# Performance work log

Hardware: AMD Instinct MI355X
Metric: run time of the kernel (lower is better)

Reference implementation:

```python
import jax, jax.numpy as jnp
import numpy as np
import math

B, S, E, H = 2, 2048, 1024, 16
D = E // H
# neuromodulator levels (deterministic branch choices)
NA, ACH, DA = 0.5, 0.5, -0.5

def setup_inputs() -> dict:
    key = jax.random.key(0)
    ks = jax.random.split(key, 12)
    xav = lambda k, i, o: jax.random.uniform(k, (i, o), jnp.float32, -1.0, 1.0) * math.sqrt(6.0 / (i + o))
    return {
        'query': jax.random.normal(ks[0], (B, S, E), jnp.float32),
        'key':   jax.random.normal(ks[1], (B, S, E), jnp.float32),
        'value': jax.random.normal(ks[2], (B, S, E), jnp.float32),
        'Wq': xav(ks[3], E, E), 'bq': jnp.zeros((E,), jnp.float32),
        'Wk': xav(ks[4], E, E), 'bk': jnp.zeros((E,), jnp.float32),
        'Wv': xav(ks[5], E, E), 'bv': jnp.zeros((E,), jnp.float32),
        'Wo': xav(ks[6], E, E), 'bo': jnp.zeros((E,), jnp.float32),
        'time_scales': jnp.ones((H,), jnp.float32),
    }

def reference(query, key, value, Wq, bq, Wk, bk, Wv, bv, Wo, bo, time_scales):
    # projections -> [B, H, S, D]
    q = (query @ Wq + bq).reshape(B, S, H, D).transpose(0, 2, 1, 3)
    k = (key   @ Wk + bk).reshape(B, S, H, D).transpose(0, 2, 1, 3)
    v = (value @ Wv + bv).reshape(B, S, H, D).transpose(0, 2, 1, 3)
    # per-head time-scale on keys
    k = k * time_scales[None, :, None, None]
    scores = jnp.einsum('bhtd,bhsd->bhts', q, k) / math.sqrt(D)
    # noradrenaline: temperature scaling
    temperature = 1.0 / (1.0 + NA * 0.5)
    scores = scores / temperature
    # acetylcholine: boost diagonal
    diag = jnp.eye(S, dtype=scores.dtype)[None, None]
    scores = scores * (1.0 + ACH * 0.3 * diag)
    kk = max(1, int(S * 0.2))
    topv = jax.lax.top_k(scores, kk)[0]          # [B,H,S,kk]
    min_topk = topv[..., -1:]                     # kth largest
    mask = (scores >= min_topk).astype(scores.dtype)
    scores = scores * (1.0 + (-DA) * 0.3 * mask)
    attn = jax.nn.softmax(scores, axis=-1)
    out = jnp.einsum('bhts,bhsd->bhtd', attn, v)
    out = out.transpose(0, 2, 1, 3).reshape(B, S, E)
    out = out @ Wo + bo
    return out
```

## Files before the change

kernel.cpp:

```cpp
#include <hip/hip_runtime.h>
#include <cstdint>
#include <cstddef>

#define BB 2
#define SS 2048
#define EE 1024
#define HH 16
#define DH 64
#define KKSEL 409
#define QT 16
#define PST 136

typedef __attribute__((ext_vector_type(8))) short bf16x8;
typedef __attribute__((ext_vector_type(4))) float f32x4;
typedef unsigned short ushort_t;

__device__ __forceinline__ unsigned short f2bf(float f){
    unsigned u = __float_as_uint(f);
    u += 0x7fffu + ((u >> 16) & 1u);
    return (unsigned short)(u >> 16);
}
__device__ __forceinline__ float bf2f(unsigned short h){
    return __uint_as_float(((unsigned)h) << 16);
}
__device__ __forceinline__ unsigned sortkey(float f){
    unsigned u = __float_as_uint(f);
    return (u & 0x80000000u) ? ~u : (u | 0x80000000u);
}
__device__ __forceinline__ float inv_sortkey(unsigned k){
    unsigned u = (k & 0x80000000u) ? (k & 0x7fffffffu) : ~k;
    return __uint_as_float(u);
}
__device__ __forceinline__ void split8(const float* f, bf16x8& h, bf16x8& l){
    #pragma unroll
    for (int j = 0; j < 8; ++j){
        ushort_t hh = f2bf(f[j]);
        h[j] = (short)hh;
        l[j] = (short)f2bf(f[j] - bf2f(hh));
    }
}
__device__ __forceinline__ void gload_lds16(const ushort_t* g, ushort_t* l){
    __builtin_amdgcn_global_load_lds(
        (const __attribute__((address_space(1))) void*)g,
        (__attribute__((address_space(3))) void*)l, 16, 0, 0);
}

struct CvtArgs {
    const float* W[4];
    ushort_t* H[4];
    ushort_t* L[4];
};

__global__ __launch_bounds__(256) void convert_wt4(CvtArgs a)
{
    __shared__ float T[64][65];
    const int z = blockIdx.z;
    const float* __restrict__ W = a.W[z];
    ushort_t* __restrict__ Ht = a.H[z];
    ushort_t* __restrict__ Lt = a.L[z];

    const int tid = threadIdx.x;
    const int ty = tid >> 4, tx = tid & 15;
    const int n0 = blockIdx.x * 64, k0 = blockIdx.y * 64;
    #pragma unroll
    for (int i = 0; i < 4; ++i){
        const int kl = ty + i * 16;
        float4 w = *(const float4*)&W[(size_t)(k0 + kl) * EE + n0 + tx * 4];
        T[kl][tx*4 + 0] = w.x; T[kl][tx*4 + 1] = w.y;
        T[kl][tx*4 + 2] = w.z; T[kl][tx*4 + 3] = w.w;
    }
    __syncthreads();
    #pragma unroll
    for (int i = 0; i < 4; ++i){
        const int nl = ty + i * 16;
        ushort4 h, l;
        ushort_t* hp = &h.x; ushort_t* lp = &l.x;
        #pragma unroll
        for (int j = 0; j < 4; ++j){
            const float v = T[tx*4 + j][nl];
            ushort_t hh = f2bf(v);
            hp[j] = hh;
            lp[j] = f2bf(v - bf2f(hh));
        }
        const size_t o = (size_t)(n0 + nl) * EE + k0 + tx * 4;
        *(ushort4*)&Ht[o] = h;
        *(ushort4*)&Lt[o] = l;
    }
}

template<int MODE>
__device__ __forceinline__ void gemm_body(
        const float* __restrict__ X,
        const ushort_t* __restrict__ Wth, const ushort_t* __restrict__ Wtl,
        const float* __restrict__ bias, const float* __restrict__ ts,
        float* __restrict__ OutF, ushort_t* __restrict__ OutH,
        ushort_t* __restrict__ OutL, ushort_t* buf, int bx, int by)
{
    const int tid  = threadIdx.x;
    const int lane = tid & 63, wave = tid >> 6;
    const int c16  = lane & 15, qd = lane >> 4;
    const int m0 = by * 128, n0 = bx * 64;
    const int wm = (wave >> 1) * 64, wn = (wave & 1) * 32;
    const int lrow = tid >> 1, lkg = (tid & 1) * 16;

    f32x4 acc[8];
    #pragma unroll
    for (int i = 0; i < 8; ++i) acc[i] = (f32x4){0.f,0.f,0.f,0.f};

    const float* Xr = X + (size_t)(m0 + lrow) * EE + lkg;

    const size_t wofs = (size_t)(n0 + wave*16 + (lane >> 2)) * EE + (lane & 3) * 8;
    const ushort_t* Wh = Wth + wofs;
    const ushort_t* Wl = Wtl + wofs;

    for (int k0 = 0; k0 < EE; k0 += 32){
        gload_lds16(Wh + k0, buf + 8192  + wave*512);
        gload_lds16(Wl + k0, buf + 10240 + wave*512);
        {
            float fx[16];
            const float* xp = Xr + k0;
            *(float4*)&fx[0]  = *(const float4*)&xp[0];
            *(float4*)&fx[4]  = *(const float4*)&xp[4];
            *(float4*)&fx[8]  = *(const float4*)&xp[8];
            *(float4*)&fx[12] = *(const float4*)&xp[12];
            bf16x8 h0, l0, h1, l1;
            split8(fx, h0, l0); split8(fx + 8, h1, l1);
            *(bf16x8*)&buf[lrow*32 + lkg]           = h0;
            *(bf16x8*)&buf[lrow*32 + lkg + 8]       = h1;
            *(bf16x8*)&buf[4096 + lrow*32 + lkg]    = l0;
            *(bf16x8*)&buf[4096 + lrow*32 + lkg+8]  = l1;
        }
        __syncthreads();

        const ushort_t* A0 = buf;
        const ushort_t* A1 = buf + 4096;
        const ushort_t* B0 = buf + 8192;
        const ushort_t* B1 = buf + 10240;
        bf16x8 afh[4], afl[4], bfh[2], bfl[2];
        #pragma unroll
        for (int i = 0; i < 4; ++i){
            afh[i] = *(const bf16x8*)&A0[(wm + i*16 + c16)*32 + qd*8];
            afl[i] = *(const bf16x8*)&A1[(wm + i*16 + c16)*32 + qd*8];
        }
        #pragma unroll
        for (int j = 0; j < 2; ++j){
            bfh[j] = *(const bf16x8*)&B0[(wn + j*16 + c16)*32 + qd*8];
            bfl[j] = *(const bf16x8*)&B1[(wn + j*16 + c16)*32 + qd*8];
        }
        if (MODE == 2){
            #pragma unroll
            for (int ma = 0; ma < 4; ++ma){
                #pragma unroll
                for (int nb = 0; nb < 2; ++nb){
                    const int id = ma*2 + nb;
                    acc[id] = __builtin_amdgcn_mfma_f32_16x16x32_bf16(afh[ma], bfh[nb], acc[id], 0,0,0);
                    acc[id] = __builtin_amdgcn_mfma_f32_16x16x32_bf16(afh[ma], bfl[nb], acc[id], 0,0,0);
                    acc[id] = __builtin_amdgcn_mfma_f32_16x16x32_bf16(afl[ma], bfh[nb], acc[id], 0,0,0);
                }
            }
        } else {
            #pragma unroll
            for (int na = 0; na < 2; ++na){
                #pragma unroll
                for (int mb = 0; mb < 4; ++mb){
                    const int id = na*4 + mb;
                    acc[id] = __builtin_amdgcn_mfma_f32_16x16x32_bf16(bfh[na], afh[mb], acc[id], 0,0,0);
                    acc[id] = __builtin_amdgcn_mfma_f32_16x16x32_bf16(bfh[na], afl[mb], acc[id], 0,0,0);
                    acc[id] = __builtin_amdgcn_mfma_f32_16x16x32_bf16(bfl[na], afh[mb], acc[id], 0,0,0);
                }
            }
        }
        if (k0 + 32 < EE) __syncthreads();
    }

    if (MODE == 3){
        #pragma unroll
        for (int na = 0; na < 2; ++na){
            const int ng = n0 + wn + na*16 + qd*4;
            float4 b4 = *(const float4*)&bias[ng];
            const float bb[4] = {b4.x, b4.y, b4.z, b4.w};
            #pragma unroll
            for (int mb = 0; mb < 4; ++mb){
                const int mg = m0 + wm + mb*16 + c16;
                const f32x4 av = acc[na*4 + mb];
                float4 o;
                o.x = av[0] + bb[0]; o.y = av[1] + bb[1];
                o.z = av[2] + bb[2]; o.w = av[3] + bb[3];
                *(float4*)&OutF[(size_t)mg * EE + ng] = o;
            }
        }
    } else if (MODE == 0){
        #pragma unroll
        for (int na = 0; na < 2; ++na){
            const int ng = n0 + wn + na*16 + qd*4;
            const int h = ng >> 6, d0 = ng & 63;
            float4 b4 = *(const float4*)&bias[ng];
            const float bb[4] = {b4.x, b4.y, b4.z, b4.w};
            #pragma unroll
            for (int mb = 0; mb < 4; ++mb){
                const int mg = m0 + wm + mb*16 + c16;
                const int bi = mg >> 11, s = mg & (SS - 1);
                const f32x4 av = acc[na*4 + mb];
                ushort4 hv, lv;
                ushort_t* hp = &hv.x; ushort_t* lp = &lv.x;
                #pragma unroll
                for (int r = 0; r < 4; ++r){
                    const float v = av[r] + bb[r];
                    ushort_t hh = f2bf(v);
                    hp[r] = hh;
                    lp[r] = f2bf(v - bf2f(hh));
                }
                const size_t o = (((size_t)(bi * HH + h)) * SS + s) * DH + d0;
                *(ushort4*)&OutH[o] = hv;
                *(ushort4*)&OutL[o] = lv;
            }
        }
    } else if (MODE == 1){
        #pragma unroll
        for (int na = 0; na < 2; ++na){
            const int ng = n0 + wn + na*16 + qd*4;
            const int h = ng >> 6, d0 = ng & 63;
            const float tsc = ts[h];
            float4 b4 = *(const float4*)&bias[ng];
            const float bb[4] = {b4.x, b4.y, b4.z, b4.w};
            #pragma unroll
            for (int mb = 0; mb < 4; ++mb){
                const int mg = m0 + wm + mb*16 + c16;
                const int bi = mg >> 11, s = mg & (SS - 1);
                const f32x4 av = acc[na*4 + mb];
                ushort4 hv;
                ushort_t* hp = &hv.x;
                #pragma unroll
                for (int r = 0; r < 4; ++r)
                    hp[r] = f2bf((av[r] + bb[r]) * tsc);
                *(ushort4*)&OutH[(((size_t)(bi * HH + h)) * SS + s) * DH + d0] = hv;
            }
        }
    } else {
        #pragma unroll
        for (int ma = 0; ma < 4; ++ma){
            const int mg = m0 + wm + ma*16 + qd*4;
            const int bi = mg >> 11, s0 = mg & (SS - 1);
            #pragma unroll
            for (int nb = 0; nb < 2; ++nb){
                const int ng = n0 + wn + nb*16 + c16;
                const int h = ng >> 6, d = ng & 63;
                const float bv = bias[ng];
                const f32x4 av = acc[ma*2 + nb];
                ushort4 hv;
                ushort_t* hp = &hv.x;
                #pragma unroll
                for (int r = 0; r < 4; ++r) hp[r] = f2bf(av[r] + bv);
                *(ushort4*)&OutH[(((size_t)(bi * HH + h)) * DH + d) * SS + s0] = hv;
            }
        }
    }
}

__device__ __forceinline__ void panel_swizzle(int& bx, int& by){
    const int lin = blockIdx.x + 16 * blockIdx.y;
    const int xcd = lin & 7, idx = lin >> 3;
    bx = idx & 15;
    by = (xcd << 2) | (idx >> 4);
}

__global__ __launch_bounds__(256) void gemm_qkv(
        const float* __restrict__ q, const float* __restrict__ k,
        const float* __restrict__ v,
        const ushort_t* __restrict__ Wqh, const ushort_t* __restrict__ Wql,
        const ushort_t* __restrict__ Wkh, const ushort_t* __restrict__ Wkl,
        const ushort_t* __restrict__ Wvh, const ushort_t* __restrict__ Wvl,
        const float* __restrict__ bq, const float* __restrict__ bk,
        const float* __restrict__ bv, const float* __restrict__ ts,
        ushort_t* __restrict__ Qh, ushort_t* __restrict__ Ql,
        ushort_t* __restrict__ Kh, ushort_t* __restrict__ Vth)
{
    __shared__ ushort_t buf[12288];
    int bx, by;
    panel_swizzle(bx, by);
    const int z = blockIdx.z;
    if (z == 0)
        gemm_body<0>(q, Wqh, Wql, bq, nullptr, nullptr, Qh, Ql, buf, bx, by);
    else if (z == 1)
        gemm_body<1>(k, Wkh, Wkl, bk, ts, nullptr, Kh, nullptr, buf, bx, by);
    else
        gemm_body<2>(v, Wvh, Wvl, bv, nullptr, nullptr, Vth, nullptr, buf, bx, by);
}

__global__ __launch_bounds__(256) void gemm_out(
        const float* __restrict__ X,
        const ushort_t* __restrict__ Wth, const ushort_t* __restrict__ Wtl,
        const float* __restrict__ bias, float* __restrict__ OutF)
{
    __shared__ ushort_t buf[12288];
    int bx, by;
    panel_swizzle(bx, by);
    gemm_body<3>(X, Wth, Wtl, bias, nullptr, OutF, nullptr, nullptr, buf, bx, by);
}

__global__ __launch_bounds__(512, 4) void attn_kernel(
        const ushort_t* __restrict__ Qh, const ushort_t* __restrict__ Ql,
        const ushort_t* __restrict__ Khi, const ushort_t* __restrict__ Vth,
        float* __restrict__ AO)
{
    __shared__ __align__(16) char uni[65536];
    __shared__ float wsums[8][16];
    __shared__ unsigned thr16[16];

    const int tid  = threadIdx.x;
    const int lane = tid & 63;
    const int wave = tid >> 6;
    const int qd   = lane >> 4;
    const int c16  = lane & 15;
    const unsigned Bx = blockIdx.x;
    const int xcd  = Bx & 7;
    const int qq   = Bx >> 3;
    const int tile = qq & 127;
    const int bh   = (qq >> 7) * 8 + xcd;
    const int t0   = tile * QT;
    const int wbase = wave * 256;

    bf16x8 qh[2], ql[2];
    {
        const size_t qbase = ((size_t)bh * SS + t0 + c16) * DH;
        #pragma unroll
        for (int kc = 0; kc < 2; ++kc){
            qh[kc] = *(const bf16x8*)&Qh[qbase + kc*32 + qd*8];
            ql[kc] = *(const bf16x8*)&Ql[qbase + kc*32 + qd*8];
        }
    }

    f32x4 acc[16];
    const ushort_t* Kh = Khi + (size_t)bh * SS * DH;
    #pragma unroll
    for (int t = 0; t < 16; ++t){
        f32x4 a = {0.f, 0.f, 0.f, 0.f};
        const int srow = wbase + t*16 + c16;
        const ushort_t* kp = Kh + (size_t)srow * DH + qd*8;
        #pragma unroll
        for (int kc = 0; kc < 2; ++kc){
            bf16x8 kh = *(const bf16x8*)(kp + kc*32);
            a = __builtin_amdgcn_mfma_f32_16x16x32_bf16(qh[kc], kh, a, 0, 0, 0);
            a = __builtin_amdgcn_mfma_f32_16x16x32_bf16(ql[kc], kh, a, 0, 0, 0);
        }
        acc[t] = a;
    }

    #pragma unroll
    for (int t = 0; t < 16; ++t){
        const int colg = wbase + t*16 + c16;
        #pragma unroll
        for (int r = 0; r < 4; ++r){
            float v = acc[t][r] * 0.15625f;
            if (colg == t0 + qd*4 + r) v *= 1.15f;
            acc[t][r] = __uint_as_float(sortkey(v));
        }
    }

    float* ex = (float*)uni;
    #pragma unroll
    for (int half = 0; half < 2; ++half){
        if ((qd >> 1) == half){
            const int rl = (qd & 1) * 4;
            #pragma unroll
            for (int t = 0; t < 16; ++t)
                #pragma unroll
                for (int r = 0; r < 4; ++r)
                    ex[(rl + r) * SS + wbase + t*16 + c16] = acc[t][r];
        }
        __syncthreads();
        unsigned cand[32];
        #pragma unroll
        for (int j = 0; j < 32; ++j)
            cand[j] = __float_as_uint(ex[wave * SS + lane + 64*j]);
        unsigned kmn = cand[0], kmx = cand[0];
        #pragma unroll
        for (int j = 1; j < 32; ++j){
            kmn = (cand[j] < kmn) ? cand[j] : kmn;
            kmx = (cand[j] > kmx) ? cand[j] : kmx;
        }
        #pragma unroll
        for (int off = 1; off < 64; off <<= 1){
            const unsigned on = (unsigned)__shfl_xor((int)kmn, off, 64);
            const unsigned ox = (unsigned)__shfl_xor((int)kmx, off, 64);
            kmn = (on < kmn) ? on : kmn;
            kmx = (ox > kmx) ? ox : kmx;
        }
        unsigned lo = kmn, hi = kmx + 1u;
        #pragma unroll 1
        for (int it = 0; it < 32 && (hi - lo) > 1u; ++it){
            const unsigned mid = lo + ((hi - lo) >> 1);
            int c = 0;
            #pragma unroll
            for (int j = 0; j < 32; ++j){
                int pc;
                asm("v_cmp_le_u32 vcc, %1, %2\n\t"
                    "s_bcnt1_i32_b64 %0, vcc"
                    : "=s"(pc) : "s"(mid), "v"(cand[j]) : "vcc");
                c += pc;
            }
            if (c == KKSEL){ lo = mid; break; }
            if (c > KKSEL) lo = mid; else hi = mid;
        }
        if (lane == 0) thr16[half*8 + wave] = lo;
        __syncthreads();
    }

    unsigned thr[4];
    #pragma unroll
    for (int r = 0; r < 4; ++r) thr[r] = thr16[qd*4 + r];
    float psum[4] = {0.f, 0.f, 0.f, 0.f};
    #pragma unroll
    for (int t = 0; t < 16; ++t){
        #pragma unroll
        for (int r = 0; r < 4; ++r){
            const unsigned key = __float_as_uint(acc[t][r]);
            float s = inv_sortkey(key);
            s *= (key >= thr[r]) ? 1.15f : 1.0f;
            const float e = __expf(s);
            acc[t][r] = e;
            psum[r] += e;
        }
    }
    #pragma unroll
    for (int off = 1; off <= 8; off <<= 1){
        #pragma unroll
        for (int r = 0; r < 4; ++r) psum[r] += __shfl_xor(psum[r], off, 64);
    }
    if (c16 == 0){
        #pragma unroll
        for (int r = 0; r < 4; ++r) wsums[wave][qd*4 + r] = psum[r];
    }
    __syncthreads();
    float pinv[4];
    #pragma unroll
    for (int r = 0; r < 4; ++r){
        const int row = qd*4 + r;
        float s = 0.f;
        #pragma unroll
        for (int w = 0; w < 8; ++w) s += wsums[w][row];
        pinv[r] = 1.f / s;
    }

    const ushort_t* Vh = Vth + (size_t)bh * DH * SS;
    ushort_t* pw = (ushort_t*)uni + wave * (QT * PST);
    f32x4 oacc[4];
    #pragma unroll
    for (int dt = 0; dt < 4; ++dt) oacc[dt] = (f32x4){0.f, 0.f, 0.f, 0.f};

    #pragma unroll
    for (int half = 0; half < 2; ++half){
        #pragma unroll
        for (int tt = 0; tt < 8; ++tt){
            const int t = half*8 + tt;
            #pragma unroll
            for (int r = 0; r < 4; ++r)
                pw[(qd*4 + r) * PST + tt*16 + c16] = f2bf(acc[t][r] * pinv[r]);
        }
        #pragma unroll
        for (int kc = 0; kc < 4; ++kc){
            bf16x8 pf = *(const bf16x8*)&pw[c16 * PST + kc*32 + qd*8];
            const int sbase = wbase + half*128 + kc*32 + qd*8;
            #pragma unroll
            for (int dt = 0; dt < 4; ++dt){
                const int d = dt*16 + c16;
                bf16x8 vh = *(const bf16x8*)(Vh + (size_t)d * SS + sbase);
                oacc[dt] = __builtin_amdgcn_mfma_f32_16x16x32_bf16(pf, vh, oacc[dt], 0, 0, 0);
            }
        }
    }

    __syncthreads();
    float* red = (float*)uni;
    #pragma unroll
    for (int dt = 0; dt < 4; ++dt)
        #pragma unroll
        for (int r = 0; r < 4; ++r)
            red[(wave*16 + qd*4 + r) * 65 + dt*16 + c16] = oacc[dt][r];
    __syncthreads();

    const int b = bh >> 4, h = bh & 15;
    {
        const int r  = tid >> 5;
        const int c2 = (tid & 31) * 2;
        float s0 = 0.f, s1 = 0.f;
        #pragma unroll
        for (int w = 0; w < 8; ++w){
            s0 += red[(w*16 + r) * 65 + c2];
            s1 += red[(w*16 + r) * 65 + c2 + 1];
        }
        float2 o; o.x = s0; o.y = s1;
        *(float2*)&AO[((size_t)b * SS + t0 + r) * EE + h*DH + c2] = o;
    }
}

extern "C" void kernel_launch(void* const* d_in, const int* in_sizes, int n_in,
                              void* d_out, int out_size, void* d_ws, size_t ws_size,
                              hipStream_t stream)
{
    const float* query = (const float*)d_in[0];
    const float* key   = (const float*)d_in[1];
    const float* value = (const float*)d_in[2];
    const float* Wq    = (const float*)d_in[3];
    const float* bq    = (const float*)d_in[4];
    const float* Wk    = (const float*)d_in[5];
    const float* bk    = (const float*)d_in[6];
    const float* Wv    = (const float*)d_in[7];
    const float* bv    = (const float*)d_in[8];
    const float* Wo    = (const float*)d_in[9];
    const float* bo    = (const float*)d_in[10];
    const float* ts    = (const float*)d_in[11];
    float* out = (float*)d_out;
    char* w = (char*)d_ws;

    const size_t MB = 1u << 20;
    ushort_t* Qh  = (ushort_t*)(w + 0 * MB);
    ushort_t* Ql  = (ushort_t*)(w + 8 * MB);
    ushort_t* Kh  = (ushort_t*)(w + 16 * MB);
    ushort_t* Vth = (ushort_t*)(w + 24 * MB);
    float*    AOw = (float*)   (w + 32 * MB);
    ushort_t* Wqh = (ushort_t*)(w + 32 * MB);
    ushort_t* Wql = (ushort_t*)(w + 34 * MB);
    ushort_t* Wkh = (ushort_t*)(w + 36 * MB);
    ushort_t* Wkl = (ushort_t*)(w + 38 * MB);
    ushort_t* Wvh = (ushort_t*)(w + 40 * MB);
    ushort_t* Wvl = (ushort_t*)(w + 42 * MB);
    ushort_t* Woh = (ushort_t*)(w + 48 * MB);
    ushort_t* Wol = (ushort_t*)(w + 50 * MB);

    CvtArgs ca;
    ca.W[0] = Wq;  ca.W[1] = Wk;  ca.W[2] = Wv;  ca.W[3] = Wo;
    ca.H[0] = Wqh; ca.H[1] = Wkh; ca.H[2] = Wvh; ca.H[3] = Woh;
    ca.L[0] = Wql; ca.L[1] = Wkl; ca.L[2] = Wvl; ca.L[3] = Wol;

    hipLaunchKernelGGL(convert_wt4, dim3(16, 16, 4), dim3(256), 0, stream, ca);
    hipLaunchKernelGGL(gemm_qkv, dim3(16, 32, 3), dim3(256), 0, stream,
                       query, key, value, Wqh, Wql, Wkh, Wkl, Wvh, Wvl,
                       bq, bk, bv, ts, Qh, Ql, Kh, Vth);
    hipLaunchKernelGGL(attn_kernel, dim3(BB * HH * (SS / QT)), dim3(512), 0, stream,
                       Qh, Ql, Kh, Vth, AOw);
    hipLaunchKernelGGL(gemm_out, dim3(16, 32), dim3(256), 0, stream,
                       AOw, Woh, Wol, bo, out);
}
```

Baseline: 663.0 us.

## Pre-split GEMM activations to bf16 hi/lo and stream them via direct LDS loads

Adds a separate pass that converts query/key/value into bf16 high/low pairs. The attention kernel now writes its output as hi/lo pairs as well. Both GEMMs then load activations with asynchronous global-to-LDS copies instead of loading fp32 into registers, splitting, and writing to LDS. This removes per-tile conversion work and the register round-trip from the GEMM inner loop, but adds an extra kernel and extra global traffic for the converted copies. It also reuses the Xq workspace region for the attention output.

```diff
diff --git a/kernel.cpp b/kernel.cpp
--- a/kernel.cpp
+++ b/kernel.cpp
@@ -88,9 +88,31 @@
     }
 }
 
+struct CvtX {
+    const float* X[3];
+    ushort_t* H[3];
+    ushort_t* L[3];
+};
+
+__global__ __launch_bounds__(256) void convert_x3(CvtX a)
+{
+    const int z = blockIdx.z;
+    const float* __restrict__ X = a.X[z];
+    ushort_t* __restrict__ Hd = a.H[z];
+    ushort_t* __restrict__ Ld = a.L[z];
+    const size_t i = ((size_t)blockIdx.x * 256 + threadIdx.x) * 8;
+    float fx[8];
+    *(float4*)&fx[0] = *(const float4*)&X[i];
+    *(float4*)&fx[4] = *(const float4*)&X[i + 4];
+    bf16x8 h, l;
+    split8(fx, h, l);
+    *(bf16x8*)&Hd[i] = h;
+    *(bf16x8*)&Ld[i] = l;
+}
+
 template<int MODE>
 __device__ __forceinline__ void gemm_body(
-        const float* __restrict__ X,
+        const ushort_t* __restrict__ Xh, const ushort_t* __restrict__ Xl,
         const ushort_t* __restrict__ Wth, const ushort_t* __restrict__ Wtl,
         const float* __restrict__ bias, const float* __restrict__ ts,
         float* __restrict__ OutF, ushort_t* __restrict__ OutH,
@@ -101,35 +123,24 @@
     const int c16  = lane & 15, qd = lane >> 4;
     const int m0 = by * 128, n0 = bx * 64;
     const int wm = (wave >> 1) * 64, wn = (wave & 1) * 32;
-    const int lrow = tid >> 1, lkg = (tid & 1) * 16;
 
     f32x4 acc[8];
     #pragma unroll
     for (int i = 0; i < 8; ++i) acc[i] = (f32x4){0.f,0.f,0.f,0.f};
 
-    const float* Xr = X + (size_t)(m0 + lrow) * EE + lkg;
-
-    const size_t wofs = (size_t)(n0 + wave*16 + (lane >> 2)) * EE + (lane & 3) * 8;
-    const ushort_t* Wh = Wth + wofs;
-    const ushort_t* Wl = Wtl + wofs;
+    const int seg0 = wave * 2, seg1 = seg0 + 1;
+    const int rl = lane >> 2, kl = (lane & 3) * 8;
+    const size_t xofs0 = (size_t)(m0 + seg0*16 + rl) * EE + kl;
+    const size_t xofs1 = (size_t)(m0 + seg1*16 + rl) * EE + kl;
+    const size_t wofs = (size_t)(n0 + wave*16 + rl) * EE + kl;
 
     for (int k0 = 0; k0 < EE; k0 += 32){
-        gload_lds16(Wh + k0, buf + 8192  + wave*512);
-        gload_lds16(Wl + k0, buf + 10240 + wave*512);
-        {
-            float fx[16];
-            const float* xp = Xr + k0;
-            *(float4*)&fx[0]  = *(const float4*)&xp[0];
-            *(float4*)&fx[4]  = *(const float4*)&xp[4];
-            *(float4*)&fx[8]  = *(const float4*)&xp[8];
-            *(float4*)&fx[12] = *(const float4*)&xp[12];
-            bf16x8 h0, l0, h1, l1;
-            split8(fx, h0, l0); split8(fx + 8, h1, l1);
-            *(bf16x8*)&buf[lrow*32 + lkg]           = h0;
-            *(bf16x8*)&buf[lrow*32 + lkg + 8]       = h1;
-            *(bf16x8*)&buf[4096 + lrow*32 + lkg]    = l0;
-            *(bf16x8*)&buf[4096 + lrow*32 + lkg+8]  = l1;
-        }
+        gload_lds16(Xh  + xofs0 + k0, buf +         seg0*512);
+        gload_lds16(Xh  + xofs1 + k0, buf +         seg1*512);
+        gload_lds16(Xl  + xofs0 + k0, buf + 4096  + seg0*512);
+        gload_lds16(Xl  + xofs1 + k0, buf + 4096  + seg1*512);
+        gload_lds16(Wth + wofs  + k0, buf + 8192  + wave*512);
+        gload_lds16(Wtl + wofs  + k0, buf + 10240 + wave*512);
         __syncthreads();
 
         const ushort_t* A0 = buf;
@@ -265,8 +276,9 @@
 }
 
 __global__ __launch_bounds__(256) void gemm_qkv(
-        const float* __restrict__ q, const float* __restrict__ k,
-        const float* __restrict__ v,
+        const ushort_t* __restrict__ Xqh, const ushort_t* __restrict__ Xql,
+        const ushort_t* __restrict__ Xkh, const ushort_t* __restrict__ Xkl,
+        const ushort_t* __restrict__ Xvh, const ushort_t* __restrict__ Xvl,
         const ushort_t* __restrict__ Wqh, const ushort_t* __restrict__ Wql,
         const ushort_t* __restrict__ Wkh, const ushort_t* __restrict__ Wkl,
         const ushort_t* __restrict__ Wvh, const ushort_t* __restrict__ Wvl,
@@ -280,28 +292,28 @@
     panel_swizzle(bx, by);
     const int z = blockIdx.z;
     if (z == 0)
-        gemm_body<0>(q, Wqh, Wql, bq, nullptr, nullptr, Qh, Ql, buf, bx, by);
+        gemm_body<0>(Xqh, Xql, Wqh, Wql, bq, nullptr, nullptr, Qh, Ql, buf, bx, by);
     else if (z == 1)
-        gemm_body<1>(k, Wkh, Wkl, bk, ts, nullptr, Kh, nullptr, buf, bx, by);
+        gemm_body<1>(Xkh, Xkl, Wkh, Wkl, bk, ts, nullptr, Kh, nullptr, buf, bx, by);
     else
-        gemm_body<2>(v, Wvh, Wvl, bv, nullptr, nullptr, Vth, nullptr, buf, bx, by);
+        gemm_body<2>(Xvh, Xvl, Wvh, Wvl, bv, nullptr, nullptr, Vth, nullptr, buf, bx, by);
 }
 
 __global__ __launch_bounds__(256) void gemm_out(
-        const float* __restrict__ X,
+        const ushort_t* __restrict__ AOh, const ushort_t* __restrict__ AOl,
         const ushort_t* __restrict__ Wth, const ushort_t* __restrict__ Wtl,
         const float* __restrict__ bias, float* __restrict__ OutF)
 {
     __shared__ ushort_t buf[12288];
     int bx, by;
     panel_swizzle(bx, by);
-    gemm_body<3>(X, Wth, Wtl, bias, nullptr, OutF, nullptr, nullptr, buf, bx, by);
+    gemm_body<3>(AOh, AOl, Wth, Wtl, bias, nullptr, OutF, nullptr, nullptr, buf, bx, by);
 }
 
 __global__ __launch_bounds__(512, 4) void attn_kernel(
         const ushort_t* __restrict__ Qh, const ushort_t* __restrict__ Ql,
         const ushort_t* __restrict__ Khi, const ushort_t* __restrict__ Vth,
-        float* __restrict__ AO)
+        ushort_t* __restrict__ AOh, ushort_t* __restrict__ AOl)
 {
     __shared__ __align__(16) char uni[65536];
     __shared__ float wsums[8][16];
@@ -489,8 +501,12 @@
             s0 += red[(w*16 + r) * 65 + c2];
             s1 += red[(w*16 + r) * 65 + c2 + 1];
         }
-        float2 o; o.x = s0; o.y = s1;
-        *(float2*)&AO[((size_t)b * SS + t0 + r) * EE + h*DH + c2] = o;
+        const size_t o = ((size_t)b * SS + t0 + r) * EE + h*DH + c2;
+        ushort2 hv, lv;
+        hv.x = f2bf(s0); lv.x = f2bf(s0 - bf2f(hv.x));
+        hv.y = f2bf(s1); lv.y = f2bf(s1 - bf2f(hv.y));
+        *(ushort2*)&AOh[o] = hv;
+        *(ushort2*)&AOl[o] = lv;
     }
 }
 
@@ -518,27 +534,41 @@
     ushort_t* Ql  = (ushort_t*)(w + 8 * MB);
     ushort_t* Kh  = (ushort_t*)(w + 16 * MB);
     ushort_t* Vth = (ushort_t*)(w + 24 * MB);
-    float*    AOw = (float*)   (w + 32 * MB);
     ushort_t* Wqh = (ushort_t*)(w + 32 * MB);
     ushort_t* Wql = (ushort_t*)(w + 34 * MB);
     ushort_t* Wkh = (ushort_t*)(w + 36 * MB);
     ushort_t* Wkl = (ushort_t*)(w + 38 * MB);
     ushort_t* Wvh = (ushort_t*)(w + 40 * MB);
     ushort_t* Wvl = (ushort_t*)(w + 42 * MB);
-    ushort_t* Woh = (ushort_t*)(w + 48 * MB);
-    ushort_t* Wol = (ushort_t*)(w + 50 * MB);
+    ushort_t* Woh = (ushort_t*)(w + 44 * MB);
+    ushort_t* Wol = (ushort_t*)(w + 46 * MB);
+    ushort_t* Xqh = (ushort_t*)(w + 48 * MB);
+    ushort_t* Xql = (ushort_t*)(w + 56 * MB);
+    ushort_t* Xkh = (ushort_t*)(w + 64 * MB);
+    ushort_t* Xkl = (ushort_t*)(w + 72 * MB);
+    ushort_t* Xvh = (ushort_t*)(w + 80 * MB);
+    ushort_t* Xvl = (ushort_t*)(w + 88 * MB);
+    ushort_t* AOh = (ushort_t*)(w + 48 * MB);
+    ushort_t* AOl = (ushort_t*)(w + 56 * MB);
 
     CvtArgs ca;
     ca.W[0] = Wq;  ca.W[1] = Wk;  ca.W[2] = Wv;  ca.W[3] = Wo;
     ca.H[0] = Wqh; ca.H[1] = Wkh; ca.H[2] = Wvh; ca.H[3] = Woh;
     ca.L[0] = Wql; ca.L[1] = Wkl; ca.L[2] = Wvl; ca.L[3] = Wol;
 
+    CvtX cx;
+    cx.X[0] = query; cx.X[1] = key; cx.X[2] = value;
+    cx.H[0] = Xqh;   cx.H[1] = Xkh; cx.H[2] = Xvh;
+    cx.L[0] = Xql;   cx.L[1] = Xkl; cx.L[2] = Xvl;
+
     hipLaunchKernelGGL(convert_wt4, dim3(16, 16, 4), dim3(256), 0, stream, ca);
+    hipLaunchKernelGGL(convert_x3, dim3(2048, 1, 3), dim3(256), 0, stream, cx);
     hipLaunchKernelGGL(gemm_qkv, dim3(16, 32, 3), dim3(256), 0, stream,
-                       query, key, value, Wqh, Wql, Wkh, Wkl, Wvh, Wvl,
+                       Xqh, Xql, Xkh, Xkl, Xvh, Xvl,
+                       Wqh, Wql, Wkh, Wkl, Wvh, Wvl,
                        bq, bk, bv, ts, Qh, Ql, Kh, Vth);
     hipLaunchKernelGGL(attn_kernel, dim3(BB * HH * (SS / QT)), dim3(512), 0, stream,
-                       Qh, Ql, Kh, Vth, AOw);
+                       Qh, Ql, Kh, Vth, AOh, AOl);
     hipLaunchKernelGGL(gemm_out, dim3(16, 32), dim3(256), 0, stream,
-                       AOw, Woh, Wol, bo, out);
-}
+                       AOh, AOl, Woh, Wol, bo, out);
+}
```

After: 641.8 us. 3.2% less time.
